# Kernel tuning notes

Hardware: AMD Instinct MI355X
Metric: run time of the kernel (lower is better)

The kernel has to match this reference:

```python
import jax, jax.numpy as jnp
import numpy as np

# PyTorch LSTM gate order: i, f, g, o. Dropout layers are identity in eval mode.

def _lstm_step(w_ih, w_hh, b):
    def step(carry, xt):
        h, c = carry
        g = xt @ w_ih.T + h @ w_hh.T + b
        i, f, gg, o = jnp.split(g, 4, axis=-1)
        c = jax.nn.sigmoid(f) * c + jax.nn.sigmoid(i) * jnp.tanh(gg)
        h = jax.nn.sigmoid(o) * jnp.tanh(c)
        return (h, c), h
    return step


def bilstm(x, wf_ih, wf_hh, bf_ih, bf_hh, wb_ih, wb_hh, bb_ih, bb_hh):
    # x: [B, T, D] -> out: [B, T, 2H]
    B = x.shape[0]
    H = wf_hh.shape[1]
    xt = jnp.swapaxes(x, 0, 1)  # [T, B, D]
    init = (jnp.zeros((B, H), x.dtype), jnp.zeros((B, H), x.dtype))
    _, hf = jax.lax.scan(_lstm_step(wf_ih, wf_hh, bf_ih + bf_hh), init, xt)
    _, hb = jax.lax.scan(_lstm_step(wb_ih, wb_hh, bb_ih + bb_hh), init, xt[::-1])
    hb = hb[::-1]
    return jnp.swapaxes(jnp.concatenate([hf, hb], axis=-1), 0, 1)


def setup_inputs() -> dict:
    key = jax.random.key(0)
    ks = iter(jax.random.split(key, 64))
    d = {"x": jax.random.normal(next(ks), (1024, 1024, 8), jnp.float32)}
    layer_dims = [(16, 20), (40, 20), (40, 10), (20, 10)]
    for li, (din, H) in enumerate(layer_dims, start=1):
        for dr in ("f", "b"):
            d[f"w{li}{dr}_ih"] = 0.1 * jax.random.normal(next(ks), (4 * H, din), jnp.float32)
            d[f"w{li}{dr}_hh"] = 0.1 * jax.random.normal(next(ks), (4 * H, H), jnp.float32)
            d[f"b{li}{dr}_ih"] = 0.1 * jax.random.normal(next(ks), (4 * H,), jnp.float32)
            d[f"b{li}{dr}_hh"] = 0.1 * jax.random.normal(next(ks), (4 * H,), jnp.float32)
    d["fc_w"] = 0.1 * jax.random.normal(next(ks), (1, 20), jnp.float32)
    d["fc_b"] = 0.1 * jax.random.normal(next(ks), (1,), jnp.float32)
    return d


def reference(x,
              w1f_ih, w1f_hh, b1f_ih, b1f_hh, w1b_ih, w1b_hh, b1b_ih, b1b_hh,
              w2f_ih, w2f_hh, b2f_ih, b2f_hh, w2b_ih, w2b_hh, b2b_ih, b2b_hh,
              w3f_ih, w3f_hh, b3f_ih, b3f_hh, w3b_ih, w3b_hh, b3b_ih, b3b_hh,
              w4f_ih, w4f_hh, b4f_ih, b4f_hh, w4b_ih, w4b_hh, b4b_ih, b4b_hh,
              fc_w, fc_b):
    # lag-1 concat: [B,T,8] -> [B,T,16]
    x_lag = jnp.concatenate([jnp.zeros_like(x[:, :1, :]), x[:, :-1, :]], axis=1)
    h = jnp.concatenate([x, x_lag], axis=2)
    h = bilstm(h, w1f_ih, w1f_hh, b1f_ih, b1f_hh, w1b_ih, w1b_hh, b1b_ih, b1b_hh)
    h = bilstm(h, w2f_ih, w2f_hh, b2f_ih, b2f_hh, w2b_ih, w2b_hh, b2b_ih, b2b_hh)
    h = bilstm(h, w3f_ih, w3f_hh, b3f_ih, b3f_hh, w3b_ih, w3b_hh, b3b_ih, b3b_hh)
    h = bilstm(h, w4f_ih, w4f_hh, b4f_ih, b4f_hh, w4b_ih, w4b_hh, b4b_ih, b4b_hh)
    h = h[:, -1, :]  # [B, 20]
    return jax.nn.sigmoid(h @ fc_w.T + fc_b)
```

## Files before the change

kernel.cpp:

```cpp
#include <hip/hip_runtime.h>
#include <hip/hip_fp16.h>
#include <stdint.h>

#define B_TOTAL 1024
#define T_TOTAL 1024
#define LOG2E 1.44269504088896f

typedef _Float16 f16x2 __attribute__((ext_vector_type(2)));

__device__ __forceinline__ float dot2acc(uint32_t xw, f16x2 w, float acc) {
#if __has_builtin(__builtin_amdgcn_fdot2)
    return __builtin_amdgcn_fdot2(__builtin_bit_cast(f16x2, xw), w, acc, false);
#else
    f16x2 xv = __builtin_bit_cast(f16x2, xw);
    return acc + (float)xv.x * (float)w.x + (float)xv.y * (float)w.y;
#endif
}

__device__ __forceinline__ uint32_t packf2(float a, float b) {
    f16x2 t;
    t.x = (_Float16)a;
    t.y = (_Float16)b;
    return __builtin_bit_cast(uint32_t, t);
}

__device__ __forceinline__ float sigm_(float z) {
    float e = __builtin_amdgcn_exp2f(-LOG2E * z);
    return __builtin_amdgcn_rcpf(1.0f + e);
}
__device__ __forceinline__ float tanh_(float z) {
    float e = __builtin_amdgcn_exp2f((2.0f * LOG2E) * z);
    float r = __builtin_amdgcn_rcpf(1.0f + e);
    return __builtin_fmaf(-2.0f, r, 1.0f);
}

__device__ __forceinline__ void wavebar() {
#if __has_builtin(__builtin_amdgcn_wave_barrier)
    __builtin_amdgcn_wave_barrier();
#endif
}

template <int D, int H, int NDIR, bool LAYER1>
__global__ void __launch_bounds__(320) gates_gemm(
    const float* __restrict__ x,
    const __half* __restrict__ inact,
    const float* __restrict__ wf, const float* __restrict__ bfi, const float* __restrict__ bfh,
    const float* __restrict__ wb, const float* __restrict__ bbi, const float* __restrict__ bbh,
    uint32_t* __restrict__ gbuf)
{
    constexpr int NG  = NDIR * 2 * H;
    constexpr int YS  = 320 / NG;
    constexpr int NDW = D / 2;

    const int tid = threadIdx.x;
    const int c   = tid % NG;
    const int s   = tid / NG;
    const int dir = c / (2 * H);
    const int rem = c % (2 * H);
    const int j   = rem >> 1;
    const int p   = rem & 1;
    const int r0  = p * 2 * H + j;
    const int r1  = r0 + H;

    const float* w  = (NDIR == 2 && dir) ? wb : wf;
    const float* bi = (NDIR == 2 && dir) ? bbi : bfi;
    const float* bh = (NDIR == 2 && dir) ? bbh : bfh;

    f16x2 w0[NDW], w1[NDW];
#pragma unroll
    for (int d = 0; d < NDW; ++d) {
        f16x2 t0, t1;
        t0.x = (_Float16)w[r0 * D + 2 * d];
        t0.y = (_Float16)w[r0 * D + 2 * d + 1];
        t1.x = (_Float16)w[r1 * D + 2 * d];
        t1.y = (_Float16)w[r1 * D + 2 * d + 1];
        w0[d] = t0;
        w1[d] = t1;
    }
    const float bias0 = bi[r0] + bh[r0];
    const float bias1 = bi[r1] + bh[r1];

    const int TB = T_TOTAL * B_TOTAL;
    for (int tb = blockIdx.x * YS + s; tb < TB; tb += gridDim.x * YS) {
        uint32_t xr[NDW];
        if constexpr (LAYER1) {
            const int t = tb >> 10;
            const int b = tb & 1023;
            const float* xp = x + ((size_t)b * T_TOTAL + t) * 8;
            float4 f0 = ((const float4*)xp)[0];
            float4 f1 = ((const float4*)xp)[1];
            float4 l0 = {0, 0, 0, 0}, l1 = {0, 0, 0, 0};
            if (t > 0) {
                l0 = ((const float4*)(xp - 8))[0];
                l1 = ((const float4*)(xp - 8))[1];
            }
            xr[0] = packf2(f0.x, f0.y); xr[1] = packf2(f0.z, f0.w);
            xr[2] = packf2(f1.x, f1.y); xr[3] = packf2(f1.z, f1.w);
            xr[4] = packf2(l0.x, l0.y); xr[5] = packf2(l0.z, l0.w);
            xr[6] = packf2(l1.x, l1.y); xr[7] = packf2(l1.z, l1.w);
        } else {
            const uint32_t* ip = (const uint32_t*)inact + (size_t)tb * NDW;
            if constexpr ((NDW % 4) == 0) {
#pragma unroll
                for (int q4 = 0; q4 < NDW / 4; ++q4) {
                    uint4 v = ((const uint4*)ip)[q4];
                    xr[4 * q4] = v.x; xr[4 * q4 + 1] = v.y;
                    xr[4 * q4 + 2] = v.z; xr[4 * q4 + 3] = v.w;
                }
            } else {
#pragma unroll
                for (int q2 = 0; q2 < NDW / 2; ++q2) {
                    uint2 v = ((const uint2*)ip)[q2];
                    xr[2 * q2] = v.x; xr[2 * q2 + 1] = v.y;
                }
                if constexpr (NDW & 1) xr[NDW - 1] = ip[NDW - 1];
            }
        }

        float d0 = bias0, d1 = bias1;
#pragma unroll
        for (int d = 0; d < NDW; ++d) {
            d0 = dot2acc(xr[d], w0[d], d0);
            d1 = dot2acc(xr[d], w1[d], d1);
        }
        gbuf[(size_t)tb * NG + c] = packf2(d0, d1);
    }
}

template <int H, int NDIR, bool STORE_ALL>
__global__ void __launch_bounds__(64, 1) lstm_scan2(
    const uint32_t* __restrict__ gbuf,
    const float* __restrict__ whhf, const float* __restrict__ whhb,
    __half* __restrict__ outact,
    float* __restrict__ lasth)
{
    constexpr int GPW   = 64 / H;
    constexpr int NH    = H / 2;
    constexpr int NG    = NDIR * 2 * H;
    constexpr int HS_DW = (H == 20) ? 12 : 8;

    const int dir  = (NDIR == 2) ? blockIdx.y : 0;
    const int lane = threadIdx.x;
    const int g    = lane / H;
    const int j    = lane - g * H;
    const int b    = blockIdx.x * GPW + g;
    const bool valid = (g < GPW) && (b < B_TOTAL);
    const int bs   = valid ? b : (B_TOTAL - 1);

    const float* w_hh = dir ? whhb : whhf;

    __shared__ uint32_t hsm[GPW + 1][HS_DW];

    f16x2 whh2[4][NH];
#pragma unroll
    for (int q = 0; q < 4; ++q) {
        const int r = q * H + j;
#pragma unroll
        for (int k = 0; k < NH; ++k) {
            f16x2 t;
            t.x = (_Float16)w_hh[r * H + 2 * k];
            t.y = (_Float16)w_hh[r * H + 2 * k + 1];
            whh2[q][k] = t;
        }
    }

    const int tstep = dir ? -1 : 1;
    const int tt0   = dir ? (T_TOTAL - 1) : 0;

    const ptrdiff_t gpstep = (ptrdiff_t)tstep * (B_TOTAL * NG);
    const uint32_t* gp = gbuf + (size_t)(tt0 * B_TOTAL + bs) * NG + dir * (2 * H) + 2 * j;

    __half* op = nullptr;
    ptrdiff_t opstep = 0;
    if constexpr (STORE_ALL) {
        op = outact + (size_t)(tt0 * B_TOTAL + bs) * (2 * H) + dir * H + j;
        opstep = (ptrdiff_t)tstep * (B_TOTAL * 2 * H);
    }

    uint2 qb[4];
#pragma unroll
    for (int s = 0; s < 3; ++s) {
        qb[s] = *(const uint2*)gp;
        gp += gpstep;
    }

    float c = 0.0f;
    float hlast = 0.0f;
    ((__half*)&hsm[g][0])[j] = __float2half(0.0f);
    wavebar();

    auto step = [&](const uint2 qc, uint2& qn, bool pf) {
        uint32_t hd[NH];
#pragma unroll
        for (int k = 0; k < NH; ++k) hd[k] = hsm[g][k];

        f16x2 lo = __builtin_bit_cast(f16x2, qc.x);
        f16x2 hi = __builtin_bit_cast(f16x2, qc.y);
        float a0 = (float)lo.x, a1 = (float)lo.y;
        float a2 = (float)hi.x, a3 = (float)hi.y;

        if (pf) { qn = *(const uint2*)gp; gp += gpstep; }

#pragma unroll
        for (int k = 0; k < NH; ++k) {
            a0 = dot2acc(hd[k], whh2[0][k], a0);
            a1 = dot2acc(hd[k], whh2[1][k], a1);
            a2 = dot2acc(hd[k], whh2[2][k], a2);
            a3 = dot2acc(hd[k], whh2[3][k], a3);
        }
        const float iv = sigm_(a0);
        const float fv = sigm_(a1);
        const float gv = tanh_(a2);
        const float ov = sigm_(a3);
        c = __builtin_fmaf(fv, c, iv * gv);
        const float h = ov * tanh_(c);
        ((__half*)&hsm[g][0])[j] = __float2half(h);
        wavebar();
        if constexpr (STORE_ALL) {
            if (valid) *op = __float2half(h);
            op += opstep;
        } else {
            hlast = h;
        }
    };

    for (int t = 0; t < T_TOTAL; t += 4) {
        step(qb[0], qb[3], t + 3 < T_TOTAL);
        step(qb[1], qb[0], t + 4 < T_TOTAL);
        step(qb[2], qb[1], t + 5 < T_TOTAL);
        step(qb[3], qb[2], t + 6 < T_TOTAL);
    }

    if constexpr (!STORE_ALL) {
        if (valid) lasth[b * H + j] = hlast;
    }
}

template <int DIN, int H, bool LAYER1, bool STORE_ALL>
__global__ void __launch_bounds__(64, 1) lstm_scan(
    const float* __restrict__ x,
    const __half* __restrict__ inbuf,
    const float* __restrict__ wihf, const float* __restrict__ whhf,
    const float* __restrict__ bihf, const float* __restrict__ bhhf,
    const float* __restrict__ wihb, const float* __restrict__ whhb,
    const float* __restrict__ bihb, const float* __restrict__ bhhb,
    __half* __restrict__ outbuf,
    float* __restrict__ lasth)
{
    constexpr int GPW   = 64 / H;
    constexpr int ND    = DIN / 2;
    constexpr int NH    = H / 2;
    constexpr int HS_DW = (H == 20) ? 12 : 8;

    const int dir  = blockIdx.y;
    const int lane = threadIdx.x;
    const int g    = lane / H;
    const int j    = lane - g * H;
    const int b    = blockIdx.x * GPW + g;
    const bool valid = (g < GPW) && (b < B_TOTAL);
    const int bs   = valid ? b : (B_TOTAL - 1);

    const float* w_ih = dir ? wihb : wihf;
    const float* w_hh = dir ? whhb : whhf;
    const float* b_ih = dir ? bihb : bihf;
    const float* b_hh = dir ? bhhb : bhhf;

    __shared__ uint32_t hsm[GPW + 1][HS_DW];

    f16x2 wih2[4][ND];
    f16x2 whh2[4][NH];
    float bias[4];
#pragma unroll
    for (int q = 0; q < 4; ++q) {
        const int r = q * H + j;
#pragma unroll
        for (int d = 0; d < ND; ++d) {
            f16x2 t;
            t.x = (_Float16)w_ih[r * DIN + 2 * d];
            t.y = (_Float16)w_ih[r * DIN + 2 * d + 1];
            wih2[q][d] = t;
        }
#pragma unroll
        for (int k = 0; k < NH; ++k) {
            f16x2 t;
            t.x = (_Float16)w_hh[r * H + 2 * k];
            t.y = (_Float16)w_hh[r * H + 2 * k + 1];
            whh2[q][k] = t;
        }
        bias[q] = b_ih[r] + b_hh[r];
    }

    const int tstep = dir ? -1 : 1;
    int tt = dir ? (T_TOTAL - 1) : 0;

    __half* op = nullptr;
    ptrdiff_t opstep = 0;
    if constexpr (STORE_ALL) {
        op = outbuf + (size_t)tt * (B_TOTAL * 2 * H) + (size_t)bs * (2 * H) + dir * H + j;
        opstep = (ptrdiff_t)tstep * (B_TOTAL * 2 * H);
    }

    float c = 0.0f;
    float hlast = 0.0f;
    ((__half*)&hsm[g][0])[j] = __float2half(0.0f);
    wavebar();

    auto tail = [&](const uint32_t* hd, float a0, float a1, float a2, float a3) {
#pragma unroll
        for (int k = 0; k < NH; ++k) {
            a0 = dot2acc(hd[k], whh2[0][k], a0);
            a1 = dot2acc(hd[k], whh2[1][k], a1);
            a2 = dot2acc(hd[k], whh2[2][k], a2);
            a3 = dot2acc(hd[k], whh2[3][k], a3);
        }
        const float iv = sigm_(a0);
        const float fv = sigm_(a1);
        const float gv = tanh_(a2);
        const float ov = sigm_(a3);
        c = __builtin_fmaf(fv, c, iv * gv);
        const float h = ov * tanh_(c);
        ((__half*)&hsm[g][0])[j] = __float2half(h);
        wavebar();
        if constexpr (STORE_ALL) {
            if (valid) *op = __float2half(h);
            op += opstep;
        } else {
            hlast = h;
        }
        tt += tstep;
    };

    if constexpr (LAYER1) {
        const float* xrow = x + (size_t)bs * (T_TOTAL * 8);
        uint32_t xcur[4], xlag[4];
        {
            const float4* p = (const float4*)(xrow + (size_t)tt * 8);
            float4 u0 = p[0], u1 = p[1];
            xcur[0] = packf2(u0.x, u0.y); xcur[1] = packf2(u0.z, u0.w);
            xcur[2] = packf2(u1.x, u1.y); xcur[3] = packf2(u1.z, u1.w);
            if (dir) {
                const float4* q = (const float4*)(xrow + (size_t)(tt - 1) * 8);
                float4 v0 = q[0], v1 = q[1];
                xlag[0] = packf2(v0.x, v0.y); xlag[1] = packf2(v0.z, v0.w);
                xlag[2] = packf2(v1.x, v1.y); xlag[3] = packf2(v1.z, v1.w);
            } else {
#pragma unroll
                for (int d = 0; d < 4; ++d) xlag[d] = 0u;
            }
        }

        for (int t = 0; t < T_TOTAL; ++t) {
            uint32_t hd[NH];
#pragma unroll
            for (int k = 0; k < NH; ++k) hd[k] = hsm[g][k];

            float a0 = bias[0], a1 = bias[1], a2 = bias[2], a3 = bias[3];
#pragma unroll
            for (int d = 0; d < 4; ++d) {
                a0 = dot2acc(xcur[d], wih2[0][d], a0);
                a1 = dot2acc(xcur[d], wih2[1][d], a1);
                a2 = dot2acc(xcur[d], wih2[2][d], a2);
                a3 = dot2acc(xcur[d], wih2[3][d], a3);
            }
#pragma unroll
            for (int d = 0; d < 4; ++d) {
                a0 = dot2acc(xlag[d], wih2[0][4 + d], a0);
                a1 = dot2acc(xlag[d], wih2[1][4 + d], a1);
                a2 = dot2acc(xlag[d], wih2[2][4 + d], a2);
                a3 = dot2acc(xlag[d], wih2[3][4 + d], a3);
            }

            const int li = dir ? (tt - 2) : (tt + 1);
            const bool ld = (li >= 0) && (li < T_TOTAL);
            float4 n0 = {0, 0, 0, 0}, n1 = {0, 0, 0, 0};
            if (ld) {
                const float4* p = (const float4*)(xrow + (size_t)li * 8);
                n0 = p[0];
                n1 = p[1];
            }

            tail(hd, a0, a1, a2, a3);

            uint32_t np[4] = {packf2(n0.x, n0.y), packf2(n0.z, n0.w),
                              packf2(n1.x, n1.y), packf2(n1.z, n1.w)};
            if (dir == 0) {
#pragma unroll
                for (int d = 0; d < 4; ++d) { xlag[d] = xcur[d]; xcur[d] = np[d]; }
            } else {
#pragma unroll
                for (int d = 0; d < 4; ++d) {
                    xcur[d] = xlag[d];
                    xlag[d] = ld ? np[d] : 0u;
                }
            }
        }
    } else {
        const ptrdiff_t ipstep = (ptrdiff_t)tstep * (B_TOTAL * ND);
        const uint32_t* ip = (const uint32_t*)inbuf + (size_t)tt * (B_TOTAL * ND) + (size_t)bs * ND;

        uint32_t xb[4][ND];
#pragma unroll
        for (int s = 0; s < 3; ++s) {
#pragma unroll
            for (int d = 0; d < ND; ++d) xb[s][d] = ip[d];
            ip += ipstep;
        }

        auto stp = [&](const uint32_t* xc, uint32_t* xn, bool pf) {
            uint32_t hd[NH];
#pragma unroll
            for (int k = 0; k < NH; ++k) hd[k] = hsm[g][k];

            float a0 = bias[0], a1 = bias[1], a2 = bias[2], a3 = bias[3];
#pragma unroll
            for (int d = 0; d < ND; ++d) {
                a0 = dot2acc(xc[d], wih2[0][d], a0);
                a1 = dot2acc(xc[d], wih2[1][d], a1);
                a2 = dot2acc(xc[d], wih2[2][d], a2);
                a3 = dot2acc(xc[d], wih2[3][d], a3);
            }
            if (pf) {
#pragma unroll
                for (int d = 0; d < ND; ++d) xn[d] = ip[d];
                ip += ipstep;
            }
            tail(hd, a0, a1, a2, a3);
        };

        for (int t = 0; t < T_TOTAL; t += 4) {
            stp(xb[0], xb[3], t + 3 < T_TOTAL);
            stp(xb[1], xb[0], t + 4 < T_TOTAL);
            stp(xb[2], xb[1], t + 5 < T_TOTAL);
            stp(xb[3], xb[2], t + 6 < T_TOTAL);
        }
    }

    if constexpr (!STORE_ALL) {
        if (valid) lasth[b * H + j] = hlast;
    }
}

__global__ void final_kernel(const __half* __restrict__ l3out,
                             const float* __restrict__ hf4,
                             const float* __restrict__ w_ih,
                             const float* __restrict__ b_ih,
                             const float* __restrict__ b_hh,
                             const float* __restrict__ fc_w,
                             const float* __restrict__ fc_b,
                             float* __restrict__ out)
{
    const int b = blockIdx.x * blockDim.x + threadIdx.x;
    if (b >= B_TOTAL) return;

    float in4[20];
    const __half* p = l3out + (size_t)(T_TOTAL - 1) * (B_TOTAL * 20) + (size_t)b * 20;
#pragma unroll
    for (int i = 0; i < 20; ++i) in4[i] = __half2float(p[i]);

    float z = fc_b[0];
#pragma unroll
    for (int k = 0; k < 10; ++k) z += fc_w[k] * hf4[b * 10 + k];

#pragma unroll
    for (int k = 0; k < 10; ++k) {
        float gi = b_ih[k]      + b_hh[k];
        float gg = b_ih[20 + k] + b_hh[20 + k];
        float go = b_ih[30 + k] + b_hh[30 + k];
#pragma unroll
        for (int i = 0; i < 20; ++i) {
            const float xi = in4[i];
            gi += w_ih[k * 20 + i]        * xi;
            gg += w_ih[(20 + k) * 20 + i] * xi;
            go += w_ih[(30 + k) * 20 + i] * xi;
        }
        const float cc = sigm_(gi) * tanh_(gg);
        const float hb = sigm_(go) * tanh_(cc);
        z += fc_w[10 + k] * hb;
    }
    out[b] = sigm_(z);
}

extern "C" void kernel_launch(void* const* d_in, const int* in_sizes, int n_in,
                              void* d_out, int out_size, void* d_ws, size_t ws_size,
                              hipStream_t stream) {
    const float* x = (const float*)d_in[0];
    auto W = [&](int li, int dr, int k) -> const float* {
        return (const float*)d_in[1 + (li - 1) * 8 + dr * 4 + k];
    };
    const float* fc_w = (const float*)d_in[33];
    const float* fc_b = (const float*)d_in[34];
    float* out = (float*)d_out;

    const size_t TB = (size_t)T_TOTAL * B_TOTAL;
    const size_t G_BYTES = TB * 80 * 4;
    const size_t A_BYTES = TB * 40 * 2;
    const size_t H4_BYTES = (size_t)B_TOTAL * 10 * 4;

    if (ws_size >= G_BYTES + A_BYTES + H4_BYTES) {
        uint32_t* G = (uint32_t*)d_ws;
        __half* A = (__half*)((char*)d_ws + G_BYTES);
        float* hf4 = (float*)((char*)d_ws + G_BYTES + A_BYTES);

        gates_gemm<16, 20, 2, true><<<2048, 320, 0, stream>>>(
            x, nullptr,
            W(1,0,0), W(1,0,2), W(1,0,3),
            W(1,1,0), W(1,1,2), W(1,1,3), G);
        lstm_scan2<20, 2, true><<<dim3(342, 2, 1), 64, 0, stream>>>(
            G, W(1,0,1), W(1,1,1), A, nullptr);

        gates_gemm<40, 20, 2, false><<<2048, 320, 0, stream>>>(
            nullptr, A,
            W(2,0,0), W(2,0,2), W(2,0,3),
            W(2,1,0), W(2,1,2), W(2,1,3), G);
        lstm_scan2<20, 2, true><<<dim3(342, 2, 1), 64, 0, stream>>>(
            G, W(2,0,1), W(2,1,1), A, nullptr);

        gates_gemm<40, 10, 2, false><<<2048, 320, 0, stream>>>(
            nullptr, A,
            W(3,0,0), W(3,0,2), W(3,0,3),
            W(3,1,0), W(3,1,2), W(3,1,3), G);
        lstm_scan2<10, 2, true><<<dim3(171, 2, 1), 64, 0, stream>>>(
            G, W(3,0,1), W(3,1,1), A, nullptr);

        gates_gemm<20, 10, 1, false><<<2048, 320, 0, stream>>>(
            nullptr, A,
            W(4,0,0), W(4,0,2), W(4,0,3),
            W(4,0,0), W(4,0,2), W(4,0,3), G);
        lstm_scan2<10, 1, false><<<dim3(171, 1, 1), 64, 0, stream>>>(
            G, W(4,0,1), W(4,0,1), nullptr, hf4);

        final_kernel<<<dim3(4, 1, 1), 256, 0, stream>>>(
            A, hf4, W(4,1,0), W(4,1,2), W(4,1,3), fc_w, fc_b, out);
    } else {
        __half* buf0 = (__half*)d_ws;
        __half* buf1 = buf0 + TB * 40;
        float* hf4 = (float*)(buf1 + TB * 40);

        lstm_scan<16, 20, true, true><<<dim3(342, 2, 1), 64, 0, stream>>>(
            x, nullptr,
            W(1,0,0), W(1,0,1), W(1,0,2), W(1,0,3),
            W(1,1,0), W(1,1,1), W(1,1,2), W(1,1,3),
            buf0, nullptr);
        lstm_scan<40, 20, false, true><<<dim3(342, 2, 1), 64, 0, stream>>>(
            nullptr, buf0,
            W(2,0,0), W(2,0,1), W(2,0,2), W(2,0,3),
            W(2,1,0), W(2,1,1), W(2,1,2), W(2,1,3),
            buf1, nullptr);
        lstm_scan<40, 10, false, true><<<dim3(171, 2, 1), 64, 0, stream>>>(
            nullptr, buf1,
            W(3,0,0), W(3,0,1), W(3,0,2), W(3,0,3),
            W(3,1,0), W(3,1,1), W(3,1,2), W(3,1,3),
            buf0, nullptr);
        lstm_scan<20, 10, false, false><<<dim3(171, 1, 1), 64, 0, stream>>>(
            nullptr, buf0,
            W(4,0,0), W(4,0,1), W(4,0,2), W(4,0,3),
            W(4,0,0), W(4,0,1), W(4,0,2), W(4,0,3),
            nullptr, hf4);
        final_kernel<<<dim3(4, 1, 1), 256, 0, stream>>>(
            buf0, hf4, W(4,1,0), W(4,1,2), W(4,1,3), fc_w, fc_b, out);
    }
}
```

Baseline: 1.742 ms.

## Chunk gate GEMM and scan over time, exchange hidden state via shuffles

Splits each bidirectional layer into time chunks, alternating a per-direction gate GEMM with a scan that carries h/c state through a small state buffer, so the gate buffer per chunk is smaller and may stay cache-resident instead of spanning the whole sequence. Each direction gets its own contiguous gate region. The scan now broadcasts h between lanes with shuffles instead of LDS plus wave barriers. Workspace offsets are hardcoded and several buffers alias each other. There are many more kernel launches, and layer 4 still uses a full-length GEMM written into an aliased region.

```diff
diff --git a/kernel.cpp b/kernel.cpp
--- a/kernel.cpp
+++ b/kernel.cpp
@@ -41,56 +41,61 @@
 }
 
 template <int D, int H, int NDIR, bool LAYER1>
-__global__ void __launch_bounds__(320) gates_gemm(
+__global__ void __launch_bounds__(320) gemmc(
     const float* __restrict__ x,
     const __half* __restrict__ inact,
     const float* __restrict__ wf, const float* __restrict__ bfi, const float* __restrict__ bfh,
     const float* __restrict__ wb, const float* __restrict__ bbi, const float* __restrict__ bbh,
-    uint32_t* __restrict__ gbuf)
+    uint32_t* __restrict__ G, int dirstride_dw, int t0_d0, int t0_d1, int tn)
 {
-    constexpr int NG  = NDIR * 2 * H;
-    constexpr int YS  = 320 / NG;
-    constexpr int NDW = D / 2;
-
+    constexpr int COLS = 2 * H;
+    constexpr int YS   = 320 / COLS;
+    constexpr int NDW  = D / 2;
+
+    const int dir = (NDIR == 2) ? blockIdx.y : 0;
     const int tid = threadIdx.x;
-    const int c   = tid % NG;
-    const int s   = tid / NG;
-    const int dir = c / (2 * H);
-    const int rem = c % (2 * H);
-    const int j   = rem >> 1;
-    const int p   = rem & 1;
+    const int c   = tid % COLS;
+    const int s   = tid / COLS;
+    const int j   = c >> 1;
+    const int p   = c & 1;
     const int r0  = p * 2 * H + j;
     const int r1  = r0 + H;
 
     const float* w  = (NDIR == 2 && dir) ? wb : wf;
     const float* bi = (NDIR == 2 && dir) ? bbi : bfi;
     const float* bh = (NDIR == 2 && dir) ? bbh : bfh;
+    const int t0  = (NDIR == 2 && dir) ? t0_d1 : t0_d0;
+    const int sgn = (NDIR == 2 && dir) ? -1 : 1;
 
     f16x2 w0[NDW], w1[NDW];
 #pragma unroll
     for (int d = 0; d < NDW; ++d) {
-        f16x2 t0, t1;
-        t0.x = (_Float16)w[r0 * D + 2 * d];
-        t0.y = (_Float16)w[r0 * D + 2 * d + 1];
-        t1.x = (_Float16)w[r1 * D + 2 * d];
-        t1.y = (_Float16)w[r1 * D + 2 * d + 1];
-        w0[d] = t0;
-        w1[d] = t1;
+        f16x2 t0v, t1v;
+        t0v.x = (_Float16)w[r0 * D + 2 * d];
+        t0v.y = (_Float16)w[r0 * D + 2 * d + 1];
+        t1v.x = (_Float16)w[r1 * D + 2 * d];
+        t1v.y = (_Float16)w[r1 * D + 2 * d + 1];
+        w0[d] = t0v;
+        w1[d] = t1v;
     }
     const float bias0 = bi[r0] + bh[r0];
     const float bias1 = bi[r1] + bh[r1];
 
-    const int TB = T_TOTAL * B_TOTAL;
-    for (int tb = blockIdx.x * YS + s; tb < TB; tb += gridDim.x * YS) {
+    uint32_t* Gd = G + (size_t)dir * dirstride_dw;
+    const int rows = tn * B_TOTAL;
+
+    for (int row = blockIdx.x * YS + s; row < rows; row += gridDim.x * YS) {
+        const int ct = row >> 10;
+        const int b  = row & 1023;
+        const int gt = t0 + sgn * ct;
+
         uint32_t xr[NDW];
         if constexpr (LAYER1) {
-            const int t = tb >> 10;
-            const int b = tb & 1023;
-            const float* xp = x + ((size_t)b * T_TOTAL + t) * 8;
+            const float* xp = x + ((size_t)b * T_TOTAL + gt) * 8;
             float4 f0 = ((const float4*)xp)[0];
             float4 f1 = ((const float4*)xp)[1];
             float4 l0 = {0, 0, 0, 0}, l1 = {0, 0, 0, 0};
-            if (t > 0) {
+            if (gt > 0) {
                 l0 = ((const float4*)(xp - 8))[0];
                 l1 = ((const float4*)(xp - 8))[1];
             }
@@ -99,7 +104,7 @@
             xr[4] = packf2(l0.x, l0.y); xr[5] = packf2(l0.z, l0.w);
             xr[6] = packf2(l1.x, l1.y); xr[7] = packf2(l1.z, l1.w);
         } else {
-            const uint32_t* ip = (const uint32_t*)inact + (size_t)tb * NDW;
+            const uint32_t* ip = (const uint32_t*)(inact + ((size_t)gt * B_TOTAL + b) * D);
             if constexpr ((NDW % 4) == 0) {
 #pragma unroll
                 for (int q4 = 0; q4 < NDW / 4; ++q4) {
@@ -113,7 +118,6 @@
                     uint2 v = ((const uint2*)ip)[q2];
                     xr[2 * q2] = v.x; xr[2 * q2 + 1] = v.y;
                 }
-                if constexpr (NDW & 1) xr[NDW - 1] = ip[NDW - 1];
             }
         }
 
@@ -123,21 +127,22 @@
             d0 = dot2acc(xr[d], w0[d], d0);
             d1 = dot2acc(xr[d], w1[d], d1);
         }
-        gbuf[(size_t)tb * NG + c] = packf2(d0, d1);
+        Gd[(size_t)row * COLS + c] = packf2(d0, d1);
     }
 }
 
 template <int H, int NDIR, bool STORE_ALL>
-__global__ void __launch_bounds__(64, 1) lstm_scan2(
-    const uint32_t* __restrict__ gbuf,
+__global__ void __launch_bounds__(64, 1) scan2c(
+    const uint32_t* __restrict__ G, int dirstride_dw,
     const float* __restrict__ whhf, const float* __restrict__ whhb,
     __half* __restrict__ outact,
-    float* __restrict__ lasth)
+    float* __restrict__ state,
+    float* __restrict__ lasth,
+    int t0_d0, int t0_d1, int tn, int initflag)
 {
-    constexpr int GPW   = 64 / H;
-    constexpr int NH    = H / 2;
-    constexpr int NG    = NDIR * 2 * H;
-    constexpr int HS_DW = (H == 20) ? 12 : 8;
+    constexpr int GPW = 64 / H;
+    constexpr int NH  = H / 2;
+    constexpr int NGD = 2 * H;
 
     const int dir  = (NDIR == 2) ? blockIdx.y : 0;
     const int lane = threadIdx.x;
@@ -145,11 +150,12 @@
     const int j    = lane - g * H;
     const int b    = blockIdx.x * GPW + g;
     const bool valid = (g < GPW) && (b < B_TOTAL);
-    const int bs   = valid ? b : (B_TOTAL - 1);
+    const int bs    = valid ? b : (B_TOTAL - 1);
+    const int gbase = (g < GPW ? g : (GPW - 1)) * H;
 
     const float* w_hh = dir ? whhb : whhf;
-
-    __shared__ uint32_t hsm[GPW + 1][HS_DW];
+    const int t0  = dir ? t0_d1 : t0_d0;
+    const int sgn = dir ? -1 : 1;
 
     f16x2 whh2[4][NH];
 #pragma unroll
@@ -164,42 +170,43 @@
         }
     }
 
-    const int tstep = dir ? -1 : 1;
-    const int tt0   = dir ? (T_TOTAL - 1) : 0;
-
-    const ptrdiff_t gpstep = (ptrdiff_t)tstep * (B_TOTAL * NG);
-    const uint32_t* gp = gbuf + (size_t)(tt0 * B_TOTAL + bs) * NG + dir * (2 * H) + 2 * j;
+    const uint32_t* gp = G + (size_t)dir * dirstride_dw + (size_t)bs * NGD + 2 * j;
+    const size_t gstep = (size_t)B_TOTAL * NGD;
 
     __half* op = nullptr;
     ptrdiff_t opstep = 0;
     if constexpr (STORE_ALL) {
-        op = outact + (size_t)(tt0 * B_TOTAL + bs) * (2 * H) + dir * H + j;
-        opstep = (ptrdiff_t)tstep * (B_TOTAL * 2 * H);
-    }
+        op = outact + ((size_t)t0 * B_TOTAL + bs) * (2 * H) + dir * H + j;
+        opstep = (ptrdiff_t)sgn * (B_TOTAL * 2 * H);
+    }
+
+    float* sp = state + (((size_t)dir * B_TOTAL + bs) * H + j) * 2;
+    float h, c;
+    if (initflag) { h = 0.0f; c = 0.0f; }
+    else          { h = sp[0]; c = sp[1]; }
 
     uint2 qb[4];
 #pragma unroll
     for (int s = 0; s < 3; ++s) {
         qb[s] = *(const uint2*)gp;
-        gp += gpstep;
-    }
-
-    float c = 0.0f;
-    float hlast = 0.0f;
-    ((__half*)&hsm[g][0])[j] = __float2half(0.0f);
-    wavebar();
+        gp += gstep;
+    }
 
     auto step = [&](const uint2 qc, uint2& qn, bool pf) {
         uint32_t hd[NH];
 #pragma unroll
-        for (int k = 0; k < NH; ++k) hd[k] = hsm[g][k];
+        for (int k = 0; k < NH; ++k) {
+            float v0 = __shfl(h, gbase + 2 * k, 64);
+            float v1 = __shfl(h, gbase + 2 * k + 1, 64);
+            hd[k] = packf2(v0, v1);
+        }
 
         f16x2 lo = __builtin_bit_cast(f16x2, qc.x);
         f16x2 hi = __builtin_bit_cast(f16x2, qc.y);
         float a0 = (float)lo.x, a1 = (float)lo.y;
         float a2 = (float)hi.x, a3 = (float)hi.y;
 
-        if (pf) { qn = *(const uint2*)gp; gp += gpstep; }
+        if (pf) { qn = *(const uint2*)gp; gp += gstep; }
 
 #pragma unroll
         for (int k = 0; k < NH; ++k) {
@@ -213,26 +220,24 @@
         const float gv = tanh_(a2);
         const float ov = sigm_(a3);
         c = __builtin_fmaf(fv, c, iv * gv);
-        const float h = ov * tanh_(c);
-        ((__half*)&hsm[g][0])[j] = __float2half(h);
-        wavebar();
+        h = ov * tanh_(c);
         if constexpr (STORE_ALL) {
             if (valid) *op = __float2half(h);
             op += opstep;
-        } else {
-            hlast = h;
         }
     };
 
-    for (int t = 0; t < T_TOTAL; t += 4) {
-        step(qb[0], qb[3], t + 3 < T_TOTAL);
-        step(qb[1], qb[0], t + 4 < T_TOTAL);
-        step(qb[2], qb[1], t + 5 < T_TOTAL);
-        step(qb[3], qb[2], t + 6 < T_TOTAL);
-    }
-
-    if constexpr (!STORE_ALL) {
-        if (valid) lasth[b * H + j] = hlast;
+    for (int t = 0; t < tn; t += 4) {
+        step(qb[0], qb[3], t + 3 < tn);
+        step(qb[1], qb[0], t + 4 < tn);
+        step(qb[2], qb[1], t + 5 < tn);
+        step(qb[3], qb[2], t + 6 < tn);
+    }
+
+    if constexpr (STORE_ALL) {
+        if (valid) { sp[0] = h; sp[1] = c; }
+    } else {
+        if (valid) lasth[b * H + j] = h;
     }
 }
 
@@ -330,71 +335,7 @@
         tt += tstep;
     };
 
-    if constexpr (LAYER1) {
-        const float* xrow = x + (size_t)bs * (T_TOTAL * 8);
-        uint32_t xcur[4], xlag[4];
-        {
-            const float4* p = (const float4*)(xrow + (size_t)tt * 8);
-            float4 u0 = p[0], u1 = p[1];
-            xcur[0] = packf2(u0.x, u0.y); xcur[1] = packf2(u0.z, u0.w);
-            xcur[2] = packf2(u1.x, u1.y); xcur[3] = packf2(u1.z, u1.w);
-            if (dir) {
-                const float4* q = (const float4*)(xrow + (size_t)(tt - 1) * 8);
-                float4 v0 = q[0], v1 = q[1];
-                xlag[0] = packf2(v0.x, v0.y); xlag[1] = packf2(v0.z, v0.w);
-                xlag[2] = packf2(v1.x, v1.y); xlag[3] = packf2(v1.z, v1.w);
-            } else {
-#pragma unroll
-                for (int d = 0; d < 4; ++d) xlag[d] = 0u;
-            }
-        }
-
-        for (int t = 0; t < T_TOTAL; ++t) {
-            uint32_t hd[NH];
-#pragma unroll
-            for (int k = 0; k < NH; ++k) hd[k] = hsm[g][k];
-
-            float a0 = bias[0], a1 = bias[1], a2 = bias[2], a3 = bias[3];
-#pragma unroll
-            for (int d = 0; d < 4; ++d) {
-                a0 = dot2acc(xcur[d], wih2[0][d], a0);
-                a1 = dot2acc(xcur[d], wih2[1][d], a1);
-                a2 = dot2acc(xcur[d], wih2[2][d], a2);
-                a3 = dot2acc(xcur[d], wih2[3][d], a3);
-            }
-#pragma unroll
-            for (int d = 0; d < 4; ++d) {
-                a0 = dot2acc(xlag[d], wih2[0][4 + d], a0);
-                a1 = dot2acc(xlag[d], wih2[1][4 + d], a1);
-                a2 = dot2acc(xlag[d], wih2[2][4 + d], a2);
-                a3 = dot2acc(xlag[d], wih2[3][4 + d], a3);
-            }
-
-            const int li = dir ? (tt - 2) : (tt + 1);
-            const bool ld = (li >= 0) && (li < T_TOTAL);
-            float4 n0 = {0, 0, 0, 0}, n1 = {0, 0, 0, 0};
-            if (ld) {
-                const float4* p = (const float4*)(xrow + (size_t)li * 8);
-                n0 = p[0];
-                n1 = p[1];
-            }
-
-            tail(hd, a0, a1, a2, a3);
-
-            uint32_t np[4] = {packf2(n0.x, n0.y), packf2(n0.z, n0.w),
-                              packf2(n1.x, n1.y), packf2(n1.z, n1.w)};
-            if (dir == 0) {
-#pragma unroll
-                for (int d = 0; d < 4; ++d) { xlag[d] = xcur[d]; xcur[d] = np[d]; }
-            } else {
-#pragma unroll
-                for (int d = 0; d < 4; ++d) {
-                    xcur[d] = xlag[d];
-                    xlag[d] = ld ? np[d] : 0u;
-                }
-            }
-        }
-    } else {
+    {
         const ptrdiff_t ipstep = (ptrdiff_t)tstep * (B_TOTAL * ND);
         const uint32_t* ip = (const uint32_t*)inbuf + (size_t)tt * (B_TOTAL * ND) + (size_t)bs * ND;
 
@@ -491,72 +432,84 @@
     const float* fc_b = (const float*)d_in[34];
     float* out = (float*)d_out;
 
-    const size_t TB = (size_t)T_TOTAL * B_TOTAL;
-    const size_t G_BYTES = TB * 80 * 4;
-    const size_t A_BYTES = TB * 40 * 2;
-    const size_t H4_BYTES = (size_t)B_TOTAL * 10 * 4;
-
-    if (ws_size >= G_BYTES + A_BYTES + H4_BYTES) {
-        uint32_t* G = (uint32_t*)d_ws;
-        __half* A = (__half*)((char*)d_ws + G_BYTES);
-        float* hf4 = (float*)((char*)d_ws + G_BYTES + A_BYTES);
-
-        gates_gemm<16, 20, 2, true><<<2048, 320, 0, stream>>>(
-            x, nullptr,
-            W(1,0,0), W(1,0,2), W(1,0,3),
-            W(1,1,0), W(1,1,2), W(1,1,3), G);
-        lstm_scan2<20, 2, true><<<dim3(342, 2, 1), 64, 0, stream>>>(
-            G, W(1,0,1), W(1,1,1), A, nullptr);
-
-        gates_gemm<40, 20, 2, false><<<2048, 320, 0, stream>>>(
-            nullptr, A,
-            W(2,0,0), W(2,0,2), W(2,0,3),
-            W(2,1,0), W(2,1,2), W(2,1,3), G);
-        lstm_scan2<20, 2, true><<<dim3(342, 2, 1), 64, 0, stream>>>(
-            G, W(2,0,1), W(2,1,1), A, nullptr);
-
-        gates_gemm<40, 10, 2, false><<<2048, 320, 0, stream>>>(
-            nullptr, A,
-            W(3,0,0), W(3,0,2), W(3,0,3),
-            W(3,1,0), W(3,1,2), W(3,1,3), G);
-        lstm_scan2<10, 2, true><<<dim3(171, 2, 1), 64, 0, stream>>>(
-            G, W(3,0,1), W(3,1,1), A, nullptr);
-
-        gates_gemm<20, 10, 1, false><<<2048, 320, 0, stream>>>(
-            nullptr, A,
-            W(4,0,0), W(4,0,2), W(4,0,3),
-            W(4,0,0), W(4,0,2), W(4,0,3), G);
-        lstm_scan2<10, 1, false><<<dim3(171, 1, 1), 64, 0, stream>>>(
-            G, W(4,0,1), W(4,0,1), nullptr, hf4);
-
-        final_kernel<<<dim3(4, 1, 1), 256, 0, stream>>>(
-            A, hf4, W(4,1,0), W(4,1,2), W(4,1,3), fc_w, fc_b, out);
+    constexpr size_t MB = 1ull << 20;
+    char* w8 = (char*)d_ws;
+    __half*   A0  = (__half*)w8;
+    __half*   A1  = (__half*)(w8 + 80 * MB);
+    uint32_t* G1  = (uint32_t*)(w8 + 80 * MB);
+    float*    ST1 = (float*)(w8 + 156 * MB);
+    uint32_t* G3  = (uint32_t*)(w8 + 40 * MB);
+    float*    ST3 = (float*)(w8 + 78 * MB);
+    float*    HF4 = (float*)(w8 + 79 * MB);
+    uint32_t* G4  = (uint32_t*)(w8 + 80 * MB);
+    uint32_t* G2  = (uint32_t*)(w8 + 160 * MB);
+    float*    ST2 = (float*)(w8 + 236 * MB);
+    const bool bigws = ws_size >= 238 * MB;
+
+    const int chs[5] = {240, 240, 240, 240, 64};
+
+    {
+        int t0a = 0, t0b = T_TOTAL - 1;
+        for (int i = 0; i < 5; ++i) {
+            const int tn = chs[i];
+            const int ds = tn * B_TOTAL * 40;
+            gemmc<16, 20, 2, true><<<dim3(1536, 2), 320, 0, stream>>>(
+                x, nullptr,
+                W(1,0,0), W(1,0,2), W(1,0,3),
+                W(1,1,0), W(1,1,2), W(1,1,3),
+                G1, ds, t0a, t0b, tn);
+            scan2c<20, 2, true><<<dim3(342, 2), 64, 0, stream>>>(
+                G1, ds, W(1,0,1), W(1,1,1), A0, ST1, nullptr, t0a, t0b, tn, i == 0);
+            t0a += tn; t0b -= tn;
+        }
+    }
+
+    if (bigws) {
+        int t0a = 0, t0b = T_TOTAL - 1;
+        for (int i = 0; i < 5; ++i) {
+            const int tn = chs[i];
+            const int ds = tn * B_TOTAL * 40;
+            gemmc<40, 20, 2, false><<<dim3(1536, 2), 320, 0, stream>>>(
+                nullptr, A0,
+                W(2,0,0), W(2,0,2), W(2,0,3),
+                W(2,1,0), W(2,1,2), W(2,1,3),
+                G2, ds, t0a, t0b, tn);
+            scan2c<20, 2, true><<<dim3(342, 2), 64, 0, stream>>>(
+                G2, ds, W(2,0,1), W(2,1,1), A1, ST2, nullptr, t0a, t0b, tn, i == 0);
+            t0a += tn; t0b -= tn;
+        }
     } else {
-        __half* buf0 = (__half*)d_ws;
-        __half* buf1 = buf0 + TB * 40;
-        float* hf4 = (float*)(buf1 + TB * 40);
-
-        lstm_scan<16, 20, true, true><<<dim3(342, 2, 1), 64, 0, stream>>>(
-            x, nullptr,
-            W(1,0,0), W(1,0,1), W(1,0,2), W(1,0,3),
-            W(1,1,0), W(1,1,1), W(1,1,2), W(1,1,3),
-            buf0, nullptr);
-        lstm_scan<40, 20, false, true><<<dim3(342, 2, 1), 64, 0, stream>>>(
-            nullptr, buf0,
+        lstm_scan<40, 20, false, true><<<dim3(342, 2), 64, 0, stream>>>(
+            nullptr, A0,
             W(2,0,0), W(2,0,1), W(2,0,2), W(2,0,3),
             W(2,1,0), W(2,1,1), W(2,1,2), W(2,1,3),
-            buf1, nullptr);
-        lstm_scan<40, 10, false, true><<<dim3(171, 2, 1), 64, 0, stream>>>(
-            nullptr, buf1,
-            W(3,0,0), W(3,0,1), W(3,0,2), W(3,0,3),
-            W(3,1,0), W(3,1,1), W(3,1,2), W(3,1,3),
-            buf0, nullptr);
-        lstm_scan<20, 10, false, false><<<dim3(171, 1, 1), 64, 0, stream>>>(
-            nullptr, buf0,
-            W(4,0,0), W(4,0,1), W(4,0,2), W(4,0,3),
-            W(4,0,0), W(4,0,1), W(4,0,2), W(4,0,3),
-            nullptr, hf4);
-        final_kernel<<<dim3(4, 1, 1), 256, 0, stream>>>(
-            buf0, hf4, W(4,1,0), W(4,1,2), W(4,1,3), fc_w, fc_b, out);
-    }
-}
+            A1, nullptr);
+    }
+
+    {
+        int t0a = 0, t0b = T_TOTAL - 1;
+        for (int i = 0; i < 5; ++i) {
+            const int tn = chs[i];
+            const int ds = tn * B_TOTAL * 20;
+            gemmc<40, 10, 2, false><<<dim3(1536, 2), 320, 0, stream>>>(
+                nullptr, A1,
+                W(3,0,0), W(3,0,2), W(3,0,3),
+                W(3,1,0), W(3,1,2), W(3,1,3),
+                G3, ds, t0a, t0b, tn);
+            scan2c<10, 2, true><<<dim3(171, 2), 64, 0, stream>>>(
+                G3, ds, W(3,0,1), W(3,1,1), A0, ST3, nullptr, t0a, t0b, tn, i == 0);
+            t0a += tn; t0b -= tn;
+        }
+    }
+
+    gemmc<20, 10, 1, false><<<dim3(1536, 1), 320, 0, stream>>>(
+        nullptr, A0,
+        W(4,0,0), W(4,0,2), W(4,0,3),
+        W(4,0,0), W(4,0,2), W(4,0,3),
+        G4, 0, 0, 0, T_TOTAL);
+    scan2c<10, 1, false><<<dim3(171, 1), 64, 0, stream>>>(
+        G4, 0, W(4,0,1), W(4,0,1), nullptr, HF4, HF4, 0, 0, T_TOTAL, 1);
+
+    final_kernel<<<dim3(4, 1, 1), 256, 0, stream>>>(
+        A0, HF4, W(4,1,0), W(4,1,2), W(4,1,3), fc_w, fc_b, out);
+}
```

New measurement: 2.521 ms. +44.7%, slower.
